# Kernel tuning notes

Hardware: AMD Instinct MI355X
Metric: run time of the kernel (lower is better)

Reference implementation:

```python
import jax, jax.numpy as jnp
import numpy as np

B, T, D = 2, 2048, 5120        # batch, seq_len, d_model
FD, E, S, K = 384, 32, 2, 2    # ffn_dim, n_experts, n_shared, top_k


def setup_inputs() -> dict:
    key = jax.random.key(0)
    ks = jax.random.split(key, 6)
    def init(k, shape, fan_in):
        return jax.random.normal(k, shape, jnp.float32) / np.sqrt(fan_in).astype(np.float32)
    return {
        "x": jax.random.normal(ks[0], (B, T, D), jnp.float32),
        "shared_w1": init(ks[1], (S, D, FD), D),
        "shared_b1": jnp.zeros((S, FD), jnp.float32),
        "shared_w2": init(ks[2], (S, FD, D), FD),
        "shared_b2": jnp.zeros((S, D), jnp.float32),
        "routed_w1": init(ks[3], (E, D, FD), D),
        "routed_b1": jnp.zeros((E, FD), jnp.float32),
        "routed_w2": init(ks[4], (E, FD, D), FD),
        "routed_b2": jnp.zeros((E, D), jnp.float32),
        "gate_w": init(ks[5], (D, E), D),
        "gate_b": jnp.zeros((E,), jnp.float32),
    }


def reference(x, shared_w1, shared_b1, shared_w2, shared_b2,
              routed_w1, routed_b1, routed_w2, routed_b2, gate_w, gate_b):
    gelu = lambda v: jax.nn.gelu(v, approximate=False)  # torch F.gelu default = exact erf

    # shared experts: sum of S dense FFNs
    h_s = gelu(jnp.einsum('btd,sdf->sbtf', x, shared_w1) + shared_b1[:, None, None, :])
    shared_out = jnp.einsum('sbtf,sfd->btd', h_s, shared_w2) + shared_b2.sum(0)

    # gating: softmax over experts, then top-k
    probs = jax.nn.softmax(x @ gate_w + gate_b, axis=-1)          # [B,T,E]
    topk_p, topk_i = jax.lax.top_k(probs, K)                      # [B,T,K]
    # dense per-(token,expert) combine weight (0 for non-selected experts)
    w_full = jnp.sum(jax.nn.one_hot(topk_i, E, dtype=x.dtype) * topk_p[..., None], axis=-2)  # [B,T,E]

    # routed experts computed densely; weights zero-out non-selected experts,
    # yielding identical math to the masked gather/scatter dispatch.
    h_r = gelu(jnp.einsum('btd,edf->ebtf', x, routed_w1) + routed_b1[:, None, None, :])
    g = h_r * jnp.transpose(w_full, (2, 0, 1))[..., None]         # fold weight pre-w2 (avoids [E,B,T,D])
    routed_out = (jnp.einsum('ebtf,efd->btd', g, routed_w2)
                  + jnp.einsum('bte,ed->btd', w_full, routed_b2))  # weighted bias term

    return shared_out + routed_out
```

## Files before the change

### kernel.cpp

```cpp
#include <hip/hip_runtime.h>
#include <math.h>

#define NTOK 4096
#define DM   5120
#define FD   384
#define NE   32

typedef float  f32x4  __attribute__((ext_vector_type(4)));
typedef __bf16 bf16x8 __attribute__((ext_vector_type(8)));
typedef unsigned short us2 __attribute__((ext_vector_type(2)));
typedef unsigned short us4 __attribute__((ext_vector_type(4)));
typedef unsigned short us8 __attribute__((ext_vector_type(8)));

__device__ __forceinline__ unsigned short f2bf(float f) {
  unsigned int u = __float_as_uint(f);
  u += 0x7fffu + ((u >> 16) & 1u);
  return (unsigned short)(u >> 16);
}

__device__ __forceinline__ float gelu_f(float v) {
  return 0.5f * v * (1.0f + erff(v * 0.70710678118654752f));
}

__device__ __forceinline__ bf16x8 ldf(const unsigned short* p) {
  us4 lo = *(const us4*)p;
  us4 hi = *(const us4*)(p + 4);
  us8 v = {lo[0], lo[1], lo[2], lo[3], hi[0], hi[1], hi[2], hi[3]};
  return __builtin_bit_cast(bf16x8, v);
}

__device__ __forceinline__ f32x4 mfma16(bf16x8 a, bf16x8 b, f32x4 c) {
  return __builtin_amdgcn_mfma_f32_16x16x32_bf16(a, b, c, 0, 0, 0);
}

__device__ __forceinline__ bf16x8 fragld(const unsigned short* t, int row, int g) {
  return *(const bf16x8*)(t + row * 64 + ((g ^ (row & 7)) << 3));
}
__device__ __forceinline__ void fragst(unsigned short* t, int row, int g, us8 v) {
  *(us8*)(t + row * 64 + ((g ^ (row & 7)) << 3)) = v;
}

#define OFF_LOGITS 0
#define OFF_COUNTS 524288
#define OFF_SEGC   524800
#define OFF_SEGB   525312
#define OFF_TABA   525824
#define OFF_TABR0  528896
#define OFF_TABR1  529920
#define OFF_TNS    530944
#define OFF_LISTS  531456
#define OFF_WLISTS 1580032
#define OFF_HBUF   2628608
#define WS_OLD     15260672UL

#define L_LOGITS 0UL
#define L_COUNTS 524288UL
#define L_HBASE  524544UL
#define L_TABA   524800UL
#define L_TABR0  527360UL
#define L_TABR1  528384UL
#define L_TNS    529408UL
#define L_LISTS  529536UL
#define L_WLIST  1578112UL
#define L_HBUF   2626688UL
#define L_XBF    15258752UL
#define L_W1T    57201792UL
#define L_W2ST   190895232UL
#define L_W2RT   198759552UL
#define WS_NEW   324588672UL

__global__ __launch_bounds__(256) void gate_v3(
    const float* __restrict__ x, const float* __restrict__ gw,
    const float* __restrict__ gb, float* __restrict__ logits,
    unsigned short* __restrict__ xbf)
{
  __shared__ __align__(16) char gsm[22656];
  float*  xs = (float*)gsm;
  float*  gs = (float*)(gsm + 4224);
  double* ps = (double*)(gsm + 4224);

  int tid = threadIdx.x;
  int t0 = blockIdx.x * 8;

  int col  = tid & 15;
  int row  = (tid >> 4) & 1;
  int part = tid >> 5;
  int e0 = col * 2;

  double a[4][2];
  #pragma unroll
  for (int i = 0; i < 4; ++i) { a[i][0] = 0.0; a[i][1] = 0.0; }

  int sx_r = tid >> 5;
  int sx_c = (tid & 31) * 4;
  const float* xg = x + (size_t)(t0 + sx_r) * DM + sx_c;
  unsigned short* xo = xbf + (size_t)(t0 + sx_r) * DM + sx_c;

  for (int k0 = 0; k0 < DM; k0 += 128) {
    float4 xv4 = *(const float4*)(xg + k0);
    *(float4*)&xs[sx_r * 132 + sx_c] = xv4;
    us4 hx = {f2bf(xv4.x), f2bf(xv4.y), f2bf(xv4.z), f2bf(xv4.w)};
    *(us4*)(xo + k0) = hx;
    #pragma unroll
    for (int p = 0; p < 4; ++p) {
      int idx = p * 256 + tid;
      int r = idx >> 3, q = (idx & 7) * 4;
      float4 g4 = *(const float4*)(gw + (size_t)(k0 + r) * NE + q);
      *(float4*)&gs[r * 36 + q] = g4;
    }
    __syncthreads();
    #pragma unroll
    for (int kk = 0; kk < 16; ++kk) {
      int k = part * 16 + kk;
      double g0 = (double)gs[k * 36 + e0];
      double g1 = (double)gs[k * 36 + e0 + 1];
      #pragma unroll
      for (int i = 0; i < 4; ++i) {
        double xv = (double)xs[(row * 4 + i) * 132 + k];
        a[i][0] = fma(xv, g0, a[i][0]);
        a[i][1] = fma(xv, g1, a[i][1]);
      }
    }
    __syncthreads();
  }

  #pragma unroll
  for (int i = 0; i < 4; ++i) {
    double2 v; v.x = a[i][0]; v.y = a[i][1];
    *(double2*)&ps[(size_t)part * 256 + (row * 4 + i) * 32 + e0] = v;
  }
  __syncthreads();
  {
    int t = tid >> 5, e = tid & 31;
    double s = 0.0;
    #pragma unroll
    for (int p = 0; p < 8; ++p) s += ps[(size_t)p * 256 + t * 32 + e];
    logits[(size_t)(t0 + t) * NE + e] = (float)s + gb[e];
  }
}

__global__ __launch_bounds__(256) void gate_logits_kernel(
    const float* __restrict__ x, const float* __restrict__ gw,
    const float* __restrict__ gb, float* __restrict__ logits,
    unsigned short* __restrict__ xbf)
{
  __shared__ float xs[16][33];
  __shared__ float gs[32][33];
  int tid = threadIdx.x;
  int t0 = blockIdx.x * 16;
  int r = tid >> 4;
  int e0 = (tid & 15) * 2;
  double a0 = 0.0, a1 = 0.0;
  for (int k0 = 0; k0 < DM; k0 += 32) {
    {
      int rr = tid >> 4, cc = (tid & 15) * 2;
      const float* s = x + (size_t)(t0 + rr) * DM + k0 + cc;
      float s0 = s[0], s1 = s[1];
      xs[rr][cc] = s0; xs[rr][cc + 1] = s1;
      if (xbf) {
        us2 h = {f2bf(s0), f2bf(s1)};
        *(us2*)(xbf + (size_t)(t0 + rr) * DM + k0 + cc) = h;
      }
    }
    {
      int rr = tid >> 3, cc = (tid & 7) * 4;
      float4 v = *(const float4*)(gw + (size_t)(k0 + rr) * NE + cc);
      gs[rr][cc] = v.x; gs[rr][cc + 1] = v.y; gs[rr][cc + 2] = v.z; gs[rr][cc + 3] = v.w;
    }
    __syncthreads();
    #pragma unroll
    for (int kk = 0; kk < 32; ++kk) {
      double a = (double)xs[r][kk];
      a0 += a * (double)gs[kk][e0];
      a1 += a * (double)gs[kk][e0 + 1];
    }
    __syncthreads();
  }
  logits[(size_t)(t0 + r) * NE + e0]     = (float)a0 + gb[e0];
  logits[(size_t)(t0 + r) * NE + e0 + 1] = (float)a1 + gb[e0 + 1];
}

__global__ void topk_kernel(const float* __restrict__ logits, int* __restrict__ counts,
                            int* __restrict__ lists, float* __restrict__ wlists)
{
  int t = blockIdx.x * blockDim.x + threadIdx.x;
  if (t >= NTOK) return;
  float l[32];
  const float4* lp = (const float4*)(logits + (size_t)t * NE);
  #pragma unroll
  for (int i = 0; i < 8; ++i) {
    float4 v = lp[i];
    l[i*4] = v.x; l[i*4+1] = v.y; l[i*4+2] = v.z; l[i*4+3] = v.w;
  }
  float mx = l[0];
  #pragma unroll
  for (int e = 1; e < 32; ++e) mx = fmaxf(mx, l[e]);
  float s = 0.f;
  #pragma unroll
  for (int e = 0; e < 32; ++e) s += expf(l[e] - mx);
  int i1 = 0; float b1 = l[0];
  #pragma unroll
  for (int e = 1; e < 32; ++e) if (l[e] > b1) { b1 = l[e]; i1 = e; }
  int i2 = -1; float b2 = -3.4e38f;
  #pragma unroll
  for (int e = 0; e < 32; ++e) if (e != i1 && l[e] > b2) { b2 = l[e]; i2 = e; }
  float p1 = expf(b1 - mx) / s;
  float p2 = expf(b2 - mx) / s;
  int pos = atomicAdd(&counts[i1], 1);
  lists [(size_t)i1 * NTOK + pos] = t;
  wlists[(size_t)i1 * NTOK + pos] = p1;
  pos = atomicAdd(&counts[32 + i2], 1);
  lists [(size_t)(32 + i2) * NTOK + pos] = t;
  wlists[(size_t)(32 + i2) * NTOK + pos] = p2;
}

__global__ void scan_kernel(const int* __restrict__ counts, int* __restrict__ seg_count,
                            int* __restrict__ seg_hbase, int2* __restrict__ tableA,
                            int2* __restrict__ tableR0, int2* __restrict__ tableR1,
                            int* __restrict__ tns)
{
  if (threadIdx.x != 0 || blockIdx.x != 0) return;
  seg_count[0] = NTOK; seg_hbase[0] = 0;
  seg_count[1] = NTOK; seg_hbase[1] = NTOK;
  int base = 2 * NTOK;
  for (int li = 0; li < 64; ++li) {
    int c = counts[li];
    seg_count[2 + li] = c; seg_hbase[2 + li] = base; base += c;
  }
  int nA = 0;
  for (int s = 0; s < 66; ++s) {
    int c = seg_count[s];
    for (int m0 = 0; m0 < c; m0 += 64) { tableA[nA].x = s; tableA[nA].y = m0; ++nA; }
  }
  int nR0 = 0;
  for (int li = 0; li < 32; ++li)
    for (int m0 = 0; m0 < counts[li]; m0 += 64) { tableR0[nR0].x = li; tableR0[nR0].y = m0; ++nR0; }
  int nR1 = 0;
  for (int li = 32; li < 64; ++li)
    for (int m0 = 0; m0 < counts[li]; m0 += 64) { tableR1[nR1].x = li; tableR1[nR1].y = m0; ++nR1; }
  tns[0] = nA; tns[1] = nR0; tns[2] = nR1;
}

__global__ __launch_bounds__(256) void ffn1_kernel(
    const float* __restrict__ x,
    const float* __restrict__ sw1, const float* __restrict__ sb1,
    const float* __restrict__ rw1, const float* __restrict__ rb1,
    const int* __restrict__ lists,
    const int* __restrict__ seg_count, const int* __restrict__ seg_hbase,
    const int2* __restrict__ tableA, const int* __restrict__ tns,
    unsigned short* __restrict__ hbuf)
{
  if ((int)blockIdx.x >= tns[0]) return;
  int2 ent = tableA[blockIdx.x];
  int seg = ent.x, m0 = ent.y;
  int cnt = seg_count[seg];
  int hbase = seg_hbase[seg];
  int n0 = blockIdx.y * 64;
  const float *w1, *b1;
  if (seg < 2) { w1 = sw1 + (size_t)seg * DM * FD; b1 = sb1 + (size_t)seg * FD; }
  else { int e = (seg - 2) & 31; w1 = rw1 + (size_t)e * DM * FD; b1 = rb1 + (size_t)e * FD; }
  __shared__ int toks[64];
  __shared__ unsigned short As[64][44];
  __shared__ unsigned short Bs[64][44];
  int tid = threadIdx.x;
  if (tid < 64) {
    int i = m0 + tid;
    int tk = 0;
    if (i < cnt) tk = (seg < 2) ? i : lists[(size_t)(seg - 2) * NTOK + i];
    toks[tid] = tk;
  }
  __syncthreads();
  int lane = tid & 63, wave = tid >> 6;
  int wr = (wave >> 1) * 32, wc = (wave & 1) * 32;
  int l15 = lane & 15, kb = (lane >> 4) * 8;
  f32x4 zz = {0.f, 0.f, 0.f, 0.f};
  f32x4 acc[2][2];
  #pragma unroll
  for (int i = 0; i < 2; ++i)
    #pragma unroll
    for (int j = 0; j < 2; ++j) acc[i][j] = zz;
  int ar = tid >> 2, ac = (tid & 3) * 8;
  const float* axp = x + (size_t)toks[ar] * DM + ac;
  int br = tid >> 3, bc = (tid & 7) * 8;
  const float* bwp = w1 + (size_t)br * FD + n0 + bc;
  for (int k0 = 0; k0 < DM; k0 += 32) {
    float4 a0 = *(const float4*)(axp + k0);
    float4 a1 = *(const float4*)(axp + k0 + 4);
    float4 w0 = *(const float4*)bwp;
    float4 w4 = *(const float4*)(bwp + 4);
    bwp += (size_t)32 * FD;
    us4 pa0 = {f2bf(a0.x), f2bf(a0.y), f2bf(a0.z), f2bf(a0.w)};
    us4 pa1 = {f2bf(a1.x), f2bf(a1.y), f2bf(a1.z), f2bf(a1.w)};
    *(us4*)&As[ar][ac] = pa0;
    *(us4*)&As[ar][ac + 4] = pa1;
    Bs[bc + 0][br] = f2bf(w0.x); Bs[bc + 1][br] = f2bf(w0.y);
    Bs[bc + 2][br] = f2bf(w0.z); Bs[bc + 3][br] = f2bf(w0.w);
    Bs[bc + 4][br] = f2bf(w4.x); Bs[bc + 5][br] = f2bf(w4.y);
    Bs[bc + 6][br] = f2bf(w4.z); Bs[bc + 7][br] = f2bf(w4.w);
    __syncthreads();
    bf16x8 af0 = ldf(&As[wr + l15][kb]);
    bf16x8 af1 = ldf(&As[wr + 16 + l15][kb]);
    bf16x8 bf0 = ldf(&Bs[wc + l15][kb]);
    bf16x8 bf1 = ldf(&Bs[wc + 16 + l15][kb]);
    acc[0][0] = mfma16(af0, bf0, acc[0][0]);
    acc[0][1] = mfma16(af0, bf1, acc[0][1]);
    acc[1][0] = mfma16(af1, bf0, acc[1][0]);
    acc[1][1] = mfma16(af1, bf1, acc[1][1]);
    __syncthreads();
  }
  int rb4 = (lane >> 4) * 4;
  #pragma unroll
  for (int mi = 0; mi < 2; ++mi) {
    #pragma unroll
    for (int rg = 0; rg < 4; ++rg) {
      int gi = m0 + wr + mi * 16 + rb4 + rg;
      if (gi < cnt) {
        #pragma unroll
        for (int ni = 0; ni < 2; ++ni) {
          int ncol = n0 + wc + ni * 16 + l15;
          float v = acc[mi][ni][rg] + b1[ncol];
          hbuf[(size_t)(hbase + gi) * FD + ncol] = f2bf(gelu_f(v));
        }
      }
    }
  }
}

__global__ __launch_bounds__(256) void ffn2_shared_kernel(
    const unsigned short* __restrict__ hbuf,
    const float* __restrict__ sw2, const float* __restrict__ sb2,
    float* __restrict__ out)
{
  int m0 = blockIdx.x * 64;
  int n0 = blockIdx.y * 64;
  __shared__ unsigned short As[64][44];
  __shared__ unsigned short Bs[64][44];
  int tid = threadIdx.x;
  int lane = tid & 63, wave = tid >> 6;
  int wr = (wave >> 1) * 32, wc = (wave & 1) * 32;
  int l15 = lane & 15, kb = (lane >> 4) * 8;
  f32x4 zz = {0.f, 0.f, 0.f, 0.f};
  f32x4 acc[2][2];
  #pragma unroll
  for (int i = 0; i < 2; ++i)
    #pragma unroll
    for (int j = 0; j < 2; ++j) acc[i][j] = zz;
  int ar = tid >> 2, ac = (tid & 3) * 8;
  int br = tid >> 3, bc = (tid & 7) * 8;
  const float* bwp = sw2 + (size_t)br * DM + n0 + bc;
  for (int k0 = 0; k0 < 2 * FD; k0 += 32) {
    int side = (k0 >= FD) ? 1 : 0;
    const unsigned short* ap =
        hbuf + (size_t)(side * NTOK + m0 + ar) * FD + (k0 - side * FD) + ac;
    us8 av = *(const us8*)ap;
    float4 w0 = *(const float4*)bwp;
    float4 w4 = *(const float4*)(bwp + 4);
    bwp += (size_t)32 * DM;
    us4 alo = {av[0], av[1], av[2], av[3]};
    us4 ahi = {av[4], av[5], av[6], av[7]};
    *(us4*)&As[ar][ac] = alo;
    *(us4*)&As[ar][ac + 4] = ahi;
    Bs[bc + 0][br] = f2bf(w0.x); Bs[bc + 1][br] = f2bf(w0.y);
    Bs[bc + 2][br] = f2bf(w0.z); Bs[bc + 3][br] = f2bf(w0.w);
    Bs[bc + 4][br] = f2bf(w4.x); Bs[bc + 5][br] = f2bf(w4.y);
    Bs[bc + 6][br] = f2bf(w4.z); Bs[bc + 7][br] = f2bf(w4.w);
    __syncthreads();
    bf16x8 af0 = ldf(&As[wr + l15][kb]);
    bf16x8 af1 = ldf(&As[wr + 16 + l15][kb]);
    bf16x8 bf0 = ldf(&Bs[wc + l15][kb]);
    bf16x8 bf1 = ldf(&Bs[wc + 16 + l15][kb]);
    acc[0][0] = mfma16(af0, bf0, acc[0][0]);
    acc[0][1] = mfma16(af0, bf1, acc[0][1]);
    acc[1][0] = mfma16(af1, bf0, acc[1][0]);
    acc[1][1] = mfma16(af1, bf1, acc[1][1]);
    __syncthreads();
  }
  int rb4 = (lane >> 4) * 4;
  #pragma unroll
  for (int mi = 0; mi < 2; ++mi) {
    #pragma unroll
    for (int rg = 0; rg < 4; ++rg) {
      int row = m0 + wr + mi * 16 + rb4 + rg;
      #pragma unroll
      for (int ni = 0; ni < 2; ++ni) {
        int ncol = n0 + wc + ni * 16 + l15;
        out[(size_t)row * DM + ncol] = acc[mi][ni][rg] + sb2[ncol] + sb2[DM + ncol];
      }
    }
  }
}

__global__ __launch_bounds__(256) void ffn2_routed_kernel(
    const unsigned short* __restrict__ hbuf,
    const float* __restrict__ rw2, const float* __restrict__ rb2,
    const int* __restrict__ lists, const float* __restrict__ wlists,
    const int* __restrict__ counts, const int* __restrict__ seg_hbase,
    const int2* __restrict__ tableR, const int* __restrict__ tns, int tidx,
    float* __restrict__ out)
{
  if ((int)blockIdx.x >= tns[tidx]) return;
  int2 ent = tableR[blockIdx.x];
  int li = ent.x, m0 = ent.y;
  int cnt = counts[li];
  int hbase = seg_hbase[2 + li];
  int e = li & 31;
  int n0 = blockIdx.y * 64;
  const float* w2 = rw2 + (size_t)e * FD * DM;
  const float* b2 = rb2 + (size_t)e * DM;
  __shared__ unsigned short As[64][44];
  __shared__ unsigned short Bs[64][44];
  int tid = threadIdx.x;
  int lane = tid & 63, wave = tid >> 6;
  int wr = (wave >> 1) * 32, wc = (wave & 1) * 32;
  int l15 = lane & 15, kb = (lane >> 4) * 8;
  f32x4 zz = {0.f, 0.f, 0.f, 0.f};
  f32x4 acc[2][2];
  #pragma unroll
  for (int i = 0; i < 2; ++i)
    #pragma unroll
    for (int j = 0; j < 2; ++j) acc[i][j] = zz;
  int ar = tid >> 2, ac = (tid & 3) * 8;
  const unsigned short* ap = hbuf + (size_t)(hbase + m0 + ar) * FD + ac;
  int br = tid >> 3, bc = (tid & 7) * 8;
  const float* bwp = w2 + (size_t)br * DM + n0 + bc;
  for (int k0 = 0; k0 < FD; k0 += 32) {
    us8 av = *(const us8*)(ap + k0);
    float4 w0 = *(const float4*)bwp;
    float4 w4 = *(const float4*)(bwp + 4);
    bwp += (size_t)32 * DM;
    us4 alo = {av[0], av[1], av[2], av[3]};
    us4 ahi = {av[4], av[5], av[6], av[7]};
    *(us4*)&As[ar][ac] = alo;
    *(us4*)&As[ar][ac + 4] = ahi;
    Bs[bc + 0][br] = f2bf(w0.x); Bs[bc + 1][br] = f2bf(w0.y);
    Bs[bc + 2][br] = f2bf(w0.z); Bs[bc + 3][br] = f2bf(w0.w);
    Bs[bc + 4][br] = f2bf(w4.x); Bs[bc + 5][br] = f2bf(w4.y);
    Bs[bc + 6][br] = f2bf(w4.z); Bs[bc + 7][br] = f2bf(w4.w);
    __syncthreads();
    bf16x8 af0 = ldf(&As[wr + l15][kb]);
    bf16x8 af1 = ldf(&As[wr + 16 + l15][kb]);
    bf16x8 bf0 = ldf(&Bs[wc + l15][kb]);
    bf16x8 bf1 = ldf(&Bs[wc + 16 + l15][kb]);
    acc[0][0] = mfma16(af0, bf0, acc[0][0]);
    acc[0][1] = mfma16(af0, bf1, acc[0][1]);
    acc[1][0] = mfma16(af1, bf0, acc[1][0]);
    acc[1][1] = mfma16(af1, bf1, acc[1][1]);
    __syncthreads();
  }
  int rb4 = (lane >> 4) * 4;
  #pragma unroll
  for (int mi = 0; mi < 2; ++mi) {
    #pragma unroll
    for (int rg = 0; rg < 4; ++rg) {
      int gi = m0 + wr + mi * 16 + rb4 + rg;
      if (gi < cnt) {
        int tok = lists[(size_t)li * NTOK + gi];
        float wgt = wlists[(size_t)li * NTOK + gi];
        #pragma unroll
        for (int ni = 0; ni < 2; ++ni) {
          int ncol = n0 + wc + ni * 16 + l15;
          float v = (acc[mi][ni][rg] + b2[ncol]) * wgt;
          out[(size_t)tok * DM + ncol] += v;
        }
      }
    }
  }
}


__global__ void scan_v3(const int* __restrict__ counts, int* __restrict__ hbase_g,
                        int2* __restrict__ tableA, int2* __restrict__ tableR0,
                        int2* __restrict__ tableR1, int* __restrict__ tns)
{
  __shared__ int cnt[64], tprefA[64], tpref0[32], tpref1[32], hpref[64];
  int t = threadIdx.x;
  if (t < 64) cnt[t] = counts[t];
  __syncthreads();
  if (t == 0) {
    int hb = 2 * NTOK, ta = 128, t0 = 0, t1 = 0;
    for (int i = 0; i < 64; ++i) {
      int nt = (cnt[i] + 63) >> 6;
      hpref[i] = hb; hb += cnt[i];
      tprefA[i] = ta; ta += nt;
      if (i < 32) { tpref0[i] = t0; t0 += nt; }
      else        { tpref1[i - 32] = t1; t1 += nt; }
    }
    tns[0] = ta; tns[1] = t0; tns[2] = t1;
  }
  __syncthreads();
  if (t < 128) {
    int2 ent; ent.x = t >> 6; ent.y = (t & 63) * 64;
    tableA[t] = ent;
  }
  if (t < 64) {
    hbase_g[t] = hpref[t];
    int nt = (cnt[t] + 63) >> 6;
    for (int j = 0; j < nt; ++j) {
      int2 ent; ent.x = 2 + t; ent.y = j * 64;
      tableA[tprefA[t] + j] = ent;
      int2 entR; entR.x = t; entR.y = j * 64;
      if (t < 32) tableR0[tpref0[t] + j] = entR;
      else        tableR1[tpref1[t - 32] + j] = entR;
    }
  }
}

__global__ __launch_bounds__(256) void conv_w1_v2(
    const float* __restrict__ sw1, const float* __restrict__ rw1,
    unsigned short* __restrict__ w1T)
{
  int seg = blockIdx.x;
  int k0 = blockIdx.y * 64;
  int n0 = blockIdx.z * 64;
  const float* src = (seg < 2) ? sw1 + (size_t)seg * DM * FD
                               : rw1 + (size_t)(seg - 2) * DM * FD;
  __shared__ float ls[64][68];
  int tid = threadIdx.x;
  int r = tid >> 4, c4 = (tid & 15) * 4;
  #pragma unroll
  for (int p = 0; p < 4; ++p) {
    float4 v = *(const float4*)(src + (size_t)(k0 + r + p * 16) * FD + n0 + c4);
    *(float4*)&ls[r + p * 16][c4] = v;
  }
  __syncthreads();
  int n = tid >> 2, kseg = (tid & 3) * 16;
  unsigned short tmp[16];
  #pragma unroll
  for (int j = 0; j < 16; ++j) tmp[j] = f2bf(ls[kseg + j][n]);
  unsigned short* dst = w1T + (size_t)seg * FD * DM + (size_t)(n0 + n) * DM + k0 + kseg;
  us8 o0 = {tmp[0], tmp[1], tmp[2], tmp[3], tmp[4], tmp[5], tmp[6], tmp[7]};
  us8 o1 = {tmp[8], tmp[9], tmp[10], tmp[11], tmp[12], tmp[13], tmp[14], tmp[15]};
  *(us8*)dst = o0;
  *(us8*)(dst + 8) = o1;
}

__global__ __launch_bounds__(256) void conv_w2_v2(
    const float* __restrict__ sw2, const float* __restrict__ rw2,
    unsigned short* __restrict__ w2sT, unsigned short* __restrict__ w2rT)
{
  int e = blockIdx.x;
  int K = (e == 0) ? 2 * FD : FD;
  int k0 = blockIdx.y * 64;
  if (k0 >= K) return;
  int n0 = blockIdx.z * 64;
  const float* src = (e == 0) ? sw2 : rw2 + (size_t)(e - 1) * FD * DM;
  unsigned short* dstb = (e == 0) ? w2sT : w2rT + (size_t)(e - 1) * DM * FD;
  __shared__ float ls[64][68];
  int tid = threadIdx.x;
  int r = tid >> 4, c4 = (tid & 15) * 4;
  #pragma unroll
  for (int p = 0; p < 4; ++p) {
    float4 v = *(const float4*)(src + (size_t)(k0 + r + p * 16) * DM + n0 + c4);
    *(float4*)&ls[r + p * 16][c4] = v;
  }
  __syncthreads();
  int n = tid >> 2, kseg = (tid & 3) * 16;
  unsigned short tmp[16];
  #pragma unroll
  for (int j = 0; j < 16; ++j) tmp[j] = f2bf(ls[kseg + j][n]);
  unsigned short* dst = dstb + (size_t)(n0 + n) * K + k0 + kseg;
  us8 o0 = {tmp[0], tmp[1], tmp[2], tmp[3], tmp[4], tmp[5], tmp[6], tmp[7]};
  us8 o1 = {tmp[8], tmp[9], tmp[10], tmp[11], tmp[12], tmp[13], tmp[14], tmp[15]};
  *(us8*)dst = o0;
  *(us8*)(dst + 8) = o1;
}

__global__ __launch_bounds__(256) void ffn1_v3(
    const unsigned short* __restrict__ xbf, const unsigned short* __restrict__ w1T,
    const float* __restrict__ sb1, const float* __restrict__ rb1,
    const int* __restrict__ lists, const int* __restrict__ counts,
    const int* __restrict__ hbase_g, const int2* __restrict__ tableA,
    const int* __restrict__ tns, unsigned short* __restrict__ hbuf)
{
  if ((int)blockIdx.x >= tns[0]) return;
  int2 ent = tableA[blockIdx.x];
  int seg = ent.x, m0 = ent.y;
  int cnt, hbase, wseg;
  const float* b1;
  if (seg < 2) {
    cnt = NTOK; hbase = seg * NTOK; b1 = sb1 + seg * FD; wseg = seg;
  } else {
    int li = seg - 2;
    int e = li & 31;
    cnt = counts[li]; hbase = hbase_g[li];
    b1 = rb1 + (size_t)e * FD;
    wseg = 2 + e;
  }
  int n0 = blockIdx.y * 128;
  const unsigned short* w1 = w1T + (size_t)wseg * FD * DM;

  __shared__ int toks[64];
  __shared__ __align__(16) unsigned short As[64 * 64];
  __shared__ __align__(16) unsigned short Bs[128 * 64];

  int tid = threadIdx.x;
  if (tid < 64) {
    int i = m0 + tid;
    int tk;
    if (seg < 2) tk = (i < cnt) ? i : 0;
    else tk = (i < cnt) ? lists[(size_t)(seg - 2) * NTOK + i] : 0;
    toks[tid] = tk;
  }
  __syncthreads();

  int lane = tid & 63, wave = tid >> 6;
  int wr = (wave >> 1) * 32, wc = (wave & 1) * 64;
  int l15 = lane & 15, l4 = lane >> 4;

  f32x4 zz = {0.f, 0.f, 0.f, 0.f};
  f32x4 acc[2][4];
  #pragma unroll
  for (int i = 0; i < 2; ++i)
    #pragma unroll
    for (int j = 0; j < 4; ++j) acc[i][j] = zz;

  int ar0 = tid >> 3, ag0 = tid & 7;
  int arw[2] = {ar0, 32 + ar0};
  const unsigned short* asrc[2];
  asrc[0] = xbf + (size_t)toks[arw[0]] * DM + ag0 * 8;
  asrc[1] = xbf + (size_t)toks[arw[1]] * DM + ag0 * 8;
  const unsigned short* bsrc[4];
  int brow[4];
  #pragma unroll
  for (int p = 0; p < 4; ++p) {
    int idx = p * 256 + tid;
    brow[p] = idx >> 3;
    bsrc[p] = w1 + (size_t)(n0 + brow[p]) * DM + (idx & 7) * 8;
  }

  for (int k0 = 0; k0 < DM; k0 += 64) {
    us8 va[2], vb[4];
    #pragma unroll
    for (int p = 0; p < 2; ++p) va[p] = *(const us8*)(asrc[p] + k0);
    #pragma unroll
    for (int p = 0; p < 4; ++p) vb[p] = *(const us8*)(bsrc[p] + k0);
    #pragma unroll
    for (int p = 0; p < 2; ++p) fragst(As, arw[p], ag0, va[p]);
    #pragma unroll
    for (int p = 0; p < 4; ++p) fragst(Bs, brow[p], ag0, vb[p]);
    __syncthreads();
    #pragma unroll
    for (int kk = 0; kk < 2; ++kk) {
      bf16x8 af[2], bfr[4];
      #pragma unroll
      for (int mi = 0; mi < 2; ++mi) af[mi] = fragld(As, wr + mi * 16 + l15, kk * 4 + l4);
      #pragma unroll
      for (int ni = 0; ni < 4; ++ni) bfr[ni] = fragld(Bs, wc + ni * 16 + l15, kk * 4 + l4);
      #pragma unroll
      for (int mi = 0; mi < 2; ++mi)
        #pragma unroll
        for (int ni = 0; ni < 4; ++ni) acc[mi][ni] = mfma16(af[mi], bfr[ni], acc[mi][ni]);
    }
    __syncthreads();
  }

  int rb4 = l4 * 4;
  #pragma unroll
  for (int mi = 0; mi < 2; ++mi) {
    #pragma unroll
    for (int rg = 0; rg < 4; ++rg) {
      int gi = m0 + wr + mi * 16 + rb4 + rg;
      if (gi < cnt) {
        #pragma unroll
        for (int ni = 0; ni < 4; ++ni) {
          int ncol = n0 + wc + ni * 16 + l15;
          float v = acc[mi][ni][rg] + b1[ncol];
          hbuf[(size_t)(hbase + gi) * FD + ncol] = f2bf(gelu_f(v));
        }
      }
    }
  }
}

__global__ __launch_bounds__(256) void ffn2_shared_v2(
    const unsigned short* __restrict__ hbuf, const unsigned short* __restrict__ w2sT,
    const float* __restrict__ sb2, float* __restrict__ out)
{
  int m0 = blockIdx.x * 128;
  int n0 = blockIdx.y * 128;

  __shared__ __align__(16) unsigned short As[128 * 64];
  __shared__ __align__(16) unsigned short Bs[128 * 64];

  int tid = threadIdx.x;
  int lane = tid & 63, wave = tid >> 6;
  int wr = (wave >> 1) * 64, wc = (wave & 1) * 64;
  int l15 = lane & 15, l4 = lane >> 4;

  f32x4 zz = {0.f, 0.f, 0.f, 0.f};
  f32x4 acc[4][4];
  #pragma unroll
  for (int i = 0; i < 4; ++i)
    #pragma unroll
    for (int j = 0; j < 4; ++j) acc[i][j] = zz;

  int prow[4], pg[4];
  #pragma unroll
  for (int p = 0; p < 4; ++p) {
    int idx = p * 256 + tid;
    prow[p] = idx >> 3; pg[p] = idx & 7;
  }

  for (int k0 = 0; k0 < 2 * FD; k0 += 64) {
    int side = (k0 >= FD) ? 1 : 0;
    int kk0 = k0 - side * FD;
    us8 va[4], vb[4];
    #pragma unroll
    for (int p = 0; p < 4; ++p)
      va[p] = *(const us8*)(hbuf + (size_t)(side * NTOK + m0 + prow[p]) * FD + kk0 + pg[p] * 8);
    #pragma unroll
    for (int p = 0; p < 4; ++p)
      vb[p] = *(const us8*)(w2sT + (size_t)(n0 + prow[p]) * (2 * FD) + k0 + pg[p] * 8);
    #pragma unroll
    for (int p = 0; p < 4; ++p) fragst(As, prow[p], pg[p], va[p]);
    #pragma unroll
    for (int p = 0; p < 4; ++p) fragst(Bs, prow[p], pg[p], vb[p]);
    __syncthreads();
    #pragma unroll
    for (int kk = 0; kk < 2; ++kk) {
      bf16x8 af[4], bfr[4];
      #pragma unroll
      for (int mi = 0; mi < 4; ++mi) af[mi] = fragld(As, wr + mi * 16 + l15, kk * 4 + l4);
      #pragma unroll
      for (int ni = 0; ni < 4; ++ni) bfr[ni] = fragld(Bs, wc + ni * 16 + l15, kk * 4 + l4);
      #pragma unroll
      for (int mi = 0; mi < 4; ++mi)
        #pragma unroll
        for (int ni = 0; ni < 4; ++ni) acc[mi][ni] = mfma16(af[mi], bfr[ni], acc[mi][ni]);
    }
    __syncthreads();
  }

  int rb4 = l4 * 4;
  #pragma unroll
  for (int mi = 0; mi < 4; ++mi) {
    #pragma unroll
    for (int rg = 0; rg < 4; ++rg) {
      int row = m0 + wr + mi * 16 + rb4 + rg;
      #pragma unroll
      for (int ni = 0; ni < 4; ++ni) {
        int ncol = n0 + wc + ni * 16 + l15;
        out[(size_t)row * DM + ncol] = acc[mi][ni][rg] + sb2[ncol] + sb2[DM + ncol];
      }
    }
  }
}

__global__ __launch_bounds__(256) void ffn2_routed_v2(
    const unsigned short* __restrict__ hbuf, const unsigned short* __restrict__ w2rT,
    const float* __restrict__ rb2, const int* __restrict__ lists,
    const float* __restrict__ wlists, const int* __restrict__ counts,
    const int* __restrict__ hbase_g, const int2* __restrict__ tableR,
    const int* __restrict__ tns, int tidx, float* __restrict__ out)
{
  if ((int)blockIdx.x >= tns[tidx]) return;
  int2 ent = tableR[blockIdx.x];
  int li = ent.x, m0 = ent.y;
  int cnt = counts[li];
  int hbase = hbase_g[li];
  int e = li & 31;
  int n0 = blockIdx.y * 128;
  const unsigned short* w2 = w2rT + (size_t)e * DM * FD;

  __shared__ __align__(16) unsigned short As[64 * 64];
  __shared__ __align__(16) unsigned short Bs[128 * 64];

  int tid = threadIdx.x;
  int lane = tid & 63, wave = tid >> 6;
  int wr = (wave >> 1) * 32, wc = (wave & 1) * 64;
  int l15 = lane & 15, l4 = lane >> 4;

  f32x4 zz = {0.f, 0.f, 0.f, 0.f};
  f32x4 acc[2][4];
  #pragma unroll
  for (int i = 0; i < 2; ++i)
    #pragma unroll
    for (int j = 0; j < 4; ++j) acc[i][j] = zz;

  int ar0 = tid >> 3, ag0 = tid & 7;
  int arw[2] = {ar0, 32 + ar0};
  const unsigned short* asrc[2];
  asrc[0] = hbuf + (size_t)(hbase + m0 + arw[0]) * FD + ag0 * 8;
  asrc[1] = hbuf + (size_t)(hbase + m0 + arw[1]) * FD + ag0 * 8;
  const unsigned short* bsrc[4];
  int brow[4];
  #pragma unroll
  for (int p = 0; p < 4; ++p) {
    int idx = p * 256 + tid;
    brow[p] = idx >> 3;
    bsrc[p] = w2 + (size_t)(n0 + brow[p]) * FD + (idx & 7) * 8;
  }

  for (int k0 = 0; k0 < FD; k0 += 64) {
    us8 va[2], vb[4];
    #pragma unroll
    for (int p = 0; p < 2; ++p) va[p] = *(const us8*)(asrc[p] + k0);
    #pragma unroll
    for (int p = 0; p < 4; ++p) vb[p] = *(const us8*)(bsrc[p] + k0);
    #pragma unroll
    for (int p = 0; p < 2; ++p) fragst(As, arw[p], ag0, va[p]);
    #pragma unroll
    for (int p = 0; p < 4; ++p) fragst(Bs, brow[p], ag0, vb[p]);
    __syncthreads();
    #pragma unroll
    for (int kk = 0; kk < 2; ++kk) {
      bf16x8 af[2], bfr[4];
      #pragma unroll
      for (int mi = 0; mi < 2; ++mi) af[mi] = fragld(As, wr + mi * 16 + l15, kk * 4 + l4);
      #pragma unroll
      for (int ni = 0; ni < 4; ++ni) bfr[ni] = fragld(Bs, wc + ni * 16 + l15, kk * 4 + l4);
      #pragma unroll
      for (int mi = 0; mi < 2; ++mi)
        #pragma unroll
        for (int ni = 0; ni < 4; ++ni) acc[mi][ni] = mfma16(af[mi], bfr[ni], acc[mi][ni]);
    }
    __syncthreads();
  }

  int rb4 = l4 * 4;
  #pragma unroll
  for (int mi = 0; mi < 2; ++mi) {
    #pragma unroll
    for (int rg = 0; rg < 4; ++rg) {
      int gi = m0 + wr + mi * 16 + rb4 + rg;
      if (gi < cnt) {
        int tok = lists[(size_t)li * NTOK + gi];
        float wgt = wlists[(size_t)li * NTOK + gi];
        #pragma unroll
        for (int ni = 0; ni < 4; ++ni) {
          int ncol = n0 + wc + ni * 16 + l15;
          float v = (acc[mi][ni][rg] + rb2[(size_t)e * DM + ncol]) * wgt;
          out[(size_t)tok * DM + ncol] += v;
        }
      }
    }
  }
}

extern "C" void kernel_launch(void* const* d_in, const int* in_sizes, int n_in,
                              void* d_out, int out_size, void* d_ws, size_t ws_size,
                              hipStream_t stream) {
  const float* x   = (const float*)d_in[0];
  const float* sw1 = (const float*)d_in[1];
  const float* sb1 = (const float*)d_in[2];
  const float* sw2 = (const float*)d_in[3];
  const float* sb2 = (const float*)d_in[4];
  const float* rw1 = (const float*)d_in[5];
  const float* rb1 = (const float*)d_in[6];
  const float* rw2 = (const float*)d_in[7];
  const float* rb2 = (const float*)d_in[8];
  const float* gw  = (const float*)d_in[9];
  const float* gb  = (const float*)d_in[10];
  float* out = (float*)d_out;
  char* ws = (char*)d_ws;

  if (ws_size >= WS_NEW) {
    float* logits  = (float*)(ws + L_LOGITS);
    int* counts    = (int*)(ws + L_COUNTS);
    int* hbase_g   = (int*)(ws + L_HBASE);
    int2* tableA   = (int2*)(ws + L_TABA);
    int2* tableR0  = (int2*)(ws + L_TABR0);
    int2* tableR1  = (int2*)(ws + L_TABR1);
    int* tns       = (int*)(ws + L_TNS);
    int* lists     = (int*)(ws + L_LISTS);
    float* wlists  = (float*)(ws + L_WLIST);
    unsigned short* hbuf = (unsigned short*)(ws + L_HBUF);
    unsigned short* xbf  = (unsigned short*)(ws + L_XBF);
    unsigned short* w1T  = (unsigned short*)(ws + L_W1T);
    unsigned short* w2sT = (unsigned short*)(ws + L_W2ST);
    unsigned short* w2rT = (unsigned short*)(ws + L_W2RT);

    hipMemsetAsync(counts, 0, 64 * sizeof(int), stream);
    gate_v3<<<dim3(NTOK / 8), 256, 0, stream>>>(x, gw, gb, logits, xbf);
    topk_kernel<<<dim3(NTOK / 256), 256, 0, stream>>>(logits, counts, lists, wlists);
    scan_v3<<<1, 128, 0, stream>>>(counts, hbase_g, tableA, tableR0, tableR1, tns);
    conv_w1_v2<<<dim3(34, 80, 6), 256, 0, stream>>>(sw1, rw1, w1T);
    conv_w2_v2<<<dim3(33, 12, 80), 256, 0, stream>>>(sw2, rw2, w2sT, w2rT);
    ffn1_v3<<<dim3(320, 3), 256, 0, stream>>>(xbf, w1T, sb1, rb1, lists, counts,
                                              hbase_g, tableA, tns, hbuf);
    ffn2_shared_v2<<<dim3(32, 40), 256, 0, stream>>>(hbuf, w2sT, sb2, out);
    ffn2_routed_v2<<<dim3(128, 40), 256, 0, stream>>>(hbuf, w2rT, rb2, lists, wlists,
                                                      counts, hbase_g, tableR0, tns, 1, out);
    ffn2_routed_v2<<<dim3(128, 40), 256, 0, stream>>>(hbuf, w2rT, rb2, lists, wlists,
                                                      counts, hbase_g, tableR1, tns, 2, out);
    return;
  }

  if (ws_size < WS_OLD) return;
  float* logits   = (float*)(ws + OFF_LOGITS);
  int* counts     = (int*)(ws + OFF_COUNTS);
  int* seg_count  = (int*)(ws + OFF_SEGC);
  int* seg_hbase  = (int*)(ws + OFF_SEGB);
  int2* tableA    = (int2*)(ws + OFF_TABA);
  int2* tableR0   = (int2*)(ws + OFF_TABR0);
  int2* tableR1   = (int2*)(ws + OFF_TABR1);
  int* tns        = (int*)(ws + OFF_TNS);
  int* lists      = (int*)(ws + OFF_LISTS);
  float* wlists   = (float*)(ws + OFF_WLISTS);
  unsigned short* hbuf = (unsigned short*)(ws + OFF_HBUF);

  hipMemsetAsync(counts, 0, 64 * sizeof(int), stream);
  gate_logits_kernel<<<dim3(NTOK / 16), 256, 0, stream>>>(x, gw, gb, logits, (unsigned short*)0);
  topk_kernel<<<dim3(NTOK / 256), 256, 0, stream>>>(logits, counts, lists, wlists);
  scan_kernel<<<1, 1, 0, stream>>>(counts, seg_count, seg_hbase, tableA, tableR0, tableR1, tns);
  ffn1_kernel<<<dim3(384, 6), 256, 0, stream>>>(x, sw1, sb1, rw1, rb1, lists,
                                                seg_count, seg_hbase, tableA, tns, hbuf);
  ffn2_shared_kernel<<<dim3(64, 80), 256, 0, stream>>>(hbuf, sw2, sb2, out);
  ffn2_routed_kernel<<<dim3(128, 80), 256, 0, stream>>>(hbuf, rw2, rb2, lists, wlists,
                                                        counts, seg_hbase, tableR0, tns, 1, out);
  ffn2_routed_kernel<<<dim3(128, 80), 256, 0, stream>>>(hbuf, rw2, rb2, lists, wlists,
                                                        counts, seg_hbase, tableR1, tns, 2, out);
}
```

Measured before the change: 654.4 us.

## Double-buffer LDS tiles in FFN GEMMs and swizzle weight-conversion transposes

The three GEMM kernels (ffn1, shared ffn2, routed ffn2) now keep two LDS buffers. Each loop iteration issues the global loads for the next k-tile before the MFMA work on the current tile, then writes them to the other buffer, so each iteration needs one barrier instead of two. This is meant to hide global-load latency behind compute. The weight conversion kernels also XOR-swizzle the LDS transpose columns to reduce bank conflicts on the column reads. In exchange, LDS use doubles (up to 64KB in the shared ffn2 kernel), which may lower occupancy.

```diff
diff --git a/kernel.cpp b/kernel.cpp
--- a/kernel.cpp
+++ b/kernel.cpp
@@ -519,14 +519,16 @@
   int r = tid >> 4, c4 = (tid & 15) * 4;
   #pragma unroll
   for (int p = 0; p < 4; ++p) {
-    float4 v = *(const float4*)(src + (size_t)(k0 + r + p * 16) * FD + n0 + c4);
-    *(float4*)&ls[r + p * 16][c4] = v;
+    int row = r + p * 16;
+    float4 v = *(const float4*)(src + (size_t)(k0 + row) * FD + n0 + c4);
+    *(float4*)&ls[row][c4 ^ (((row >> 4) & 3) << 4)] = v;
   }
   __syncthreads();
   int n = tid >> 2, kseg = (tid & 3) * 16;
+  int swz = ((kseg >> 4) & 3) << 4;
   unsigned short tmp[16];
   #pragma unroll
-  for (int j = 0; j < 16; ++j) tmp[j] = f2bf(ls[kseg + j][n]);
+  for (int j = 0; j < 16; ++j) tmp[j] = f2bf(ls[kseg + j][n ^ swz]);
   unsigned short* dst = w1T + (size_t)seg * FD * DM + (size_t)(n0 + n) * DM + k0 + kseg;
   us8 o0 = {tmp[0], tmp[1], tmp[2], tmp[3], tmp[4], tmp[5], tmp[6], tmp[7]};
   us8 o1 = {tmp[8], tmp[9], tmp[10], tmp[11], tmp[12], tmp[13], tmp[14], tmp[15]};
@@ -550,14 +552,16 @@
   int r = tid >> 4, c4 = (tid & 15) * 4;
   #pragma unroll
   for (int p = 0; p < 4; ++p) {
-    float4 v = *(const float4*)(src + (size_t)(k0 + r + p * 16) * DM + n0 + c4);
-    *(float4*)&ls[r + p * 16][c4] = v;
+    int row = r + p * 16;
+    float4 v = *(const float4*)(src + (size_t)(k0 + row) * DM + n0 + c4);
+    *(float4*)&ls[row][c4 ^ (((row >> 4) & 3) << 4)] = v;
   }
   __syncthreads();
   int n = tid >> 2, kseg = (tid & 3) * 16;
+  int swz = ((kseg >> 4) & 3) << 4;
   unsigned short tmp[16];
   #pragma unroll
-  for (int j = 0; j < 16; ++j) tmp[j] = f2bf(ls[kseg + j][n]);
+  for (int j = 0; j < 16; ++j) tmp[j] = f2bf(ls[kseg + j][n ^ swz]);
   unsigned short* dst = dstb + (size_t)(n0 + n) * K + k0 + kseg;
   us8 o0 = {tmp[0], tmp[1], tmp[2], tmp[3], tmp[4], tmp[5], tmp[6], tmp[7]};
   us8 o1 = {tmp[8], tmp[9], tmp[10], tmp[11], tmp[12], tmp[13], tmp[14], tmp[15]};
@@ -590,8 +594,8 @@
   const unsigned short* w1 = w1T + (size_t)wseg * FD * DM;
 
   __shared__ int toks[64];
-  __shared__ __align__(16) unsigned short As[64 * 64];
-  __shared__ __align__(16) unsigned short Bs[128 * 64];
+  __shared__ __align__(16) unsigned short As[2][64 * 64];
+  __shared__ __align__(16) unsigned short Bs[2][128 * 64];
 
   int tid = threadIdx.x;
   if (tid < 64) {
@@ -628,30 +632,53 @@
     bsrc[p] = w1 + (size_t)(n0 + brow[p]) * DM + (idx & 7) * 8;
   }
 
+  {
+    us8 va[2], vb[4];
+    #pragma unroll
+    for (int p = 0; p < 2; ++p) va[p] = *(const us8*)(asrc[p]);
+    #pragma unroll
+    for (int p = 0; p < 4; ++p) vb[p] = *(const us8*)(bsrc[p]);
+    #pragma unroll
+    for (int p = 0; p < 2; ++p) fragst(As[0], arw[p], ag0, va[p]);
+    #pragma unroll
+    for (int p = 0; p < 4; ++p) fragst(Bs[0], brow[p], ag0, vb[p]);
+  }
+  __syncthreads();
+
+  int cur = 0;
   for (int k0 = 0; k0 < DM; k0 += 64) {
-    us8 va[2], vb[4];
-    #pragma unroll
-    for (int p = 0; p < 2; ++p) va[p] = *(const us8*)(asrc[p] + k0);
-    #pragma unroll
-    for (int p = 0; p < 4; ++p) vb[p] = *(const us8*)(bsrc[p] + k0);
-    #pragma unroll
-    for (int p = 0; p < 2; ++p) fragst(As, arw[p], ag0, va[p]);
-    #pragma unroll
-    for (int p = 0; p < 4; ++p) fragst(Bs, brow[p], ag0, vb[p]);
-    __syncthreads();
+    int nk = k0 + 64;
+    us8 va1[2], vb1[4];
+    if (nk < DM) {
+      #pragma unroll
+      for (int p = 0; p < 2; ++p) va1[p] = *(const us8*)(asrc[p] + nk);
+      #pragma unroll
+      for (int p = 0; p < 4; ++p) vb1[p] = *(const us8*)(bsrc[p] + nk);
+    }
+    const unsigned short* Ac = As[cur];
+    const unsigned short* Bc = Bs[cur];
     #pragma unroll
     for (int kk = 0; kk < 2; ++kk) {
       bf16x8 af[2], bfr[4];
       #pragma unroll
-      for (int mi = 0; mi < 2; ++mi) af[mi] = fragld(As, wr + mi * 16 + l15, kk * 4 + l4);
-      #pragma unroll
-      for (int ni = 0; ni < 4; ++ni) bfr[ni] = fragld(Bs, wc + ni * 16 + l15, kk * 4 + l4);
+      for (int mi = 0; mi < 2; ++mi) af[mi] = fragld(Ac, wr + mi * 16 + l15, kk * 4 + l4);
+      #pragma unroll
+      for (int ni = 0; ni < 4; ++ni) bfr[ni] = fragld(Bc, wc + ni * 16 + l15, kk * 4 + l4);
       #pragma unroll
       for (int mi = 0; mi < 2; ++mi)
         #pragma unroll
         for (int ni = 0; ni < 4; ++ni) acc[mi][ni] = mfma16(af[mi], bfr[ni], acc[mi][ni]);
     }
-    __syncthreads();
+    if (nk < DM) {
+      unsigned short* An = As[cur ^ 1];
+      unsigned short* Bn = Bs[cur ^ 1];
+      #pragma unroll
+      for (int p = 0; p < 2; ++p) fragst(An, arw[p], ag0, va1[p]);
+      #pragma unroll
+      for (int p = 0; p < 4; ++p) fragst(Bn, brow[p], ag0, vb1[p]);
+    }
+    __syncthreads();
+    cur ^= 1;
   }
 
   int rb4 = l4 * 4;
@@ -679,8 +706,8 @@
   int m0 = blockIdx.x * 128;
   int n0 = blockIdx.y * 128;
 
-  __shared__ __align__(16) unsigned short As[128 * 64];
-  __shared__ __align__(16) unsigned short Bs[128 * 64];
+  __shared__ __align__(16) unsigned short As[2][128 * 64];
+  __shared__ __align__(16) unsigned short Bs[2][128 * 64];
 
   int tid = threadIdx.x;
   int lane = tid & 63, wave = tid >> 6;
@@ -701,34 +728,59 @@
     prow[p] = idx >> 3; pg[p] = idx & 7;
   }
 
+  {
+    us8 va[4], vb[4];
+    #pragma unroll
+    for (int p = 0; p < 4; ++p)
+      va[p] = *(const us8*)(hbuf + (size_t)(m0 + prow[p]) * FD + pg[p] * 8);
+    #pragma unroll
+    for (int p = 0; p < 4; ++p)
+      vb[p] = *(const us8*)(w2sT + (size_t)(n0 + prow[p]) * (2 * FD) + pg[p] * 8);
+    #pragma unroll
+    for (int p = 0; p < 4; ++p) fragst(As[0], prow[p], pg[p], va[p]);
+    #pragma unroll
+    for (int p = 0; p < 4; ++p) fragst(Bs[0], prow[p], pg[p], vb[p]);
+  }
+  __syncthreads();
+
+  int cur = 0;
   for (int k0 = 0; k0 < 2 * FD; k0 += 64) {
-    int side = (k0 >= FD) ? 1 : 0;
-    int kk0 = k0 - side * FD;
-    us8 va[4], vb[4];
-    #pragma unroll
-    for (int p = 0; p < 4; ++p)
-      va[p] = *(const us8*)(hbuf + (size_t)(side * NTOK + m0 + prow[p]) * FD + kk0 + pg[p] * 8);
-    #pragma unroll
-    for (int p = 0; p < 4; ++p)
-      vb[p] = *(const us8*)(w2sT + (size_t)(n0 + prow[p]) * (2 * FD) + k0 + pg[p] * 8);
-    #pragma unroll
-    for (int p = 0; p < 4; ++p) fragst(As, prow[p], pg[p], va[p]);
-    #pragma unroll
-    for (int p = 0; p < 4; ++p) fragst(Bs, prow[p], pg[p], vb[p]);
-    __syncthreads();
+    int nk = k0 + 64;
+    us8 va1[4], vb1[4];
+    if (nk < 2 * FD) {
+      int side = (nk >= FD) ? 1 : 0;
+      int kk0 = nk - side * FD;
+      #pragma unroll
+      for (int p = 0; p < 4; ++p)
+        va1[p] = *(const us8*)(hbuf + (size_t)(side * NTOK + m0 + prow[p]) * FD + kk0 + pg[p] * 8);
+      #pragma unroll
+      for (int p = 0; p < 4; ++p)
+        vb1[p] = *(const us8*)(w2sT + (size_t)(n0 + prow[p]) * (2 * FD) + nk + pg[p] * 8);
+    }
+    const unsigned short* Ac = As[cur];
+    const unsigned short* Bc = Bs[cur];
     #pragma unroll
     for (int kk = 0; kk < 2; ++kk) {
       bf16x8 af[4], bfr[4];
       #pragma unroll
-      for (int mi = 0; mi < 4; ++mi) af[mi] = fragld(As, wr + mi * 16 + l15, kk * 4 + l4);
-      #pragma unroll
-      for (int ni = 0; ni < 4; ++ni) bfr[ni] = fragld(Bs, wc + ni * 16 + l15, kk * 4 + l4);
+      for (int mi = 0; mi < 4; ++mi) af[mi] = fragld(Ac, wr + mi * 16 + l15, kk * 4 + l4);
+      #pragma unroll
+      for (int ni = 0; ni < 4; ++ni) bfr[ni] = fragld(Bc, wc + ni * 16 + l15, kk * 4 + l4);
       #pragma unroll
       for (int mi = 0; mi < 4; ++mi)
         #pragma unroll
         for (int ni = 0; ni < 4; ++ni) acc[mi][ni] = mfma16(af[mi], bfr[ni], acc[mi][ni]);
     }
-    __syncthreads();
+    if (nk < 2 * FD) {
+      unsigned short* An = As[cur ^ 1];
+      unsigned short* Bn = Bs[cur ^ 1];
+      #pragma unroll
+      for (int p = 0; p < 4; ++p) fragst(An, prow[p], pg[p], va1[p]);
+      #pragma unroll
+      for (int p = 0; p < 4; ++p) fragst(Bn, prow[p], pg[p], vb1[p]);
+    }
+    __syncthreads();
+    cur ^= 1;
   }
 
   int rb4 = l4 * 4;
@@ -762,8 +814,8 @@
   int n0 = blockIdx.y * 128;
   const unsigned short* w2 = w2rT + (size_t)e * DM * FD;
 
-  __shared__ __align__(16) unsigned short As[64 * 64];
-  __shared__ __align__(16) unsigned short Bs[128 * 64];
+  __shared__ __align__(16) unsigned short As[2][64 * 64];
+  __shared__ __align__(16) unsigned short Bs[2][128 * 64];
 
   int tid = threadIdx.x;
   int lane = tid & 63, wave = tid >> 6;
@@ -791,30 +843,53 @@
     bsrc[p] = w2 + (size_t)(n0 + brow[p]) * FD + (idx & 7) * 8;
   }
 
+  {
+    us8 va[2], vb[4];
+    #pragma unroll
+    for (int p = 0; p < 2; ++p) va[p] = *(const us8*)(asrc[p]);
+    #pragma unroll
+    for (int p = 0; p < 4; ++p) vb[p] = *(const us8*)(bsrc[p]);
+    #pragma unroll
+    for (int p = 0; p < 2; ++p) fragst(As[0], arw[p], ag0, va[p]);
+    #pragma unroll
+    for (int p = 0; p < 4; ++p) fragst(Bs[0], brow[p], ag0, vb[p]);
+  }
+  __syncthreads();
+
+  int cur = 0;
   for (int k0 = 0; k0 < FD; k0 += 64) {
-    us8 va[2], vb[4];
-    #pragma unroll
-    for (int p = 0; p < 2; ++p) va[p] = *(const us8*)(asrc[p] + k0);
-    #pragma unroll
-    for (int p = 0; p < 4; ++p) vb[p] = *(const us8*)(bsrc[p] + k0);
-    #pragma unroll
-    for (int p = 0; p < 2; ++p) fragst(As, arw[p], ag0, va[p]);
-    #pragma unroll
-    for (int p = 0; p < 4; ++p) fragst(Bs, brow[p], ag0, vb[p]);
-    __syncthreads();
+    int nk = k0 + 64;
+    us8 va1[2], vb1[4];
+    if (nk < FD) {
+      #pragma unroll
+      for (int p = 0; p < 2; ++p) va1[p] = *(const us8*)(asrc[p] + nk);
+      #pragma unroll
+      for (int p = 0; p < 4; ++p) vb1[p] = *(const us8*)(bsrc[p] + nk);
+    }
+    const unsigned short* Ac = As[cur];
+    const unsigned short* Bc = Bs[cur];
     #pragma unroll
     for (int kk = 0; kk < 2; ++kk) {
       bf16x8 af[2], bfr[4];
       #pragma unroll
-      for (int mi = 0; mi < 2; ++mi) af[mi] = fragld(As, wr + mi * 16 + l15, kk * 4 + l4);
-      #pragma unroll
-      for (int ni = 0; ni < 4; ++ni) bfr[ni] = fragld(Bs, wc + ni * 16 + l15, kk * 4 + l4);
+      for (int mi = 0; mi < 2; ++mi) af[mi] = fragld(Ac, wr + mi * 16 + l15, kk * 4 + l4);
+      #pragma unroll
+      for (int ni = 0; ni < 4; ++ni) bfr[ni] = fragld(Bc, wc + ni * 16 + l15, kk * 4 + l4);
       #pragma unroll
       for (int mi = 0; mi < 2; ++mi)
         #pragma unroll
         for (int ni = 0; ni < 4; ++ni) acc[mi][ni] = mfma16(af[mi], bfr[ni], acc[mi][ni]);
     }
-    __syncthreads();
+    if (nk < FD) {
+      unsigned short* An = As[cur ^ 1];
+      unsigned short* Bn = Bs[cur ^ 1];
+      #pragma unroll
+      for (int p = 0; p < 2; ++p) fragst(An, arw[p], ag0, va1[p]);
+      #pragma unroll
+      for (int p = 0; p < 4; ++p) fragst(Bn, brow[p], ag0, vb1[p]);
+    }
+    __syncthreads();
+    cur ^= 1;
   }
 
   int rb4 = l4 * 4;
```

Result: slower. 689.3 us (+5.3%).

## Load GEMM tiles directly into LDS and swizzle transpose staging buffers

Applied to the files above, without the earlier changes.

The three GEMM kernels (ffn1, shared ffn2, routed ffn2) now stage A and B tiles with global_load_lds 16-byte direct-to-LDS loads instead of loading into registers and then storing to LDS. The XOR swizzle is moved to the global source address so the existing fragment reads still match. The weight-conversion transpose kernels also gain an XOR swizzle on their fp32 LDS tile to reduce bank conflicts on column reads. This is meant to cut VGPR pressure and LDS store instructions, but it relies on the builtin's per-wave destination layout being correct and still synchronises with barriers and no explicit vmcnt wait.

```diff
diff --git a/kernel.cpp b/kernel.cpp
--- a/kernel.cpp
+++ b/kernel.cpp
@@ -38,6 +38,12 @@
 }
 __device__ __forceinline__ void fragst(unsigned short* t, int row, int g, us8 v) {
   *(us8*)(t + row * 64 + ((g ^ (row & 7)) << 3)) = v;
+}
+
+__device__ __forceinline__ void gld16(const void* g, void* l) {
+  __builtin_amdgcn_global_load_lds(
+      (const __attribute__((address_space(1))) unsigned int*)g,
+      (__attribute__((address_space(3))) unsigned int*)l, 16, 0, 0);
 }
 
 #define OFF_LOGITS 0
@@ -519,14 +525,16 @@
   int r = tid >> 4, c4 = (tid & 15) * 4;
   #pragma unroll
   for (int p = 0; p < 4; ++p) {
-    float4 v = *(const float4*)(src + (size_t)(k0 + r + p * 16) * FD + n0 + c4);
-    *(float4*)&ls[r + p * 16][c4] = v;
+    int row = r + p * 16;
+    float4 v = *(const float4*)(src + (size_t)(k0 + row) * FD + n0 + c4);
+    *(float4*)&ls[row][c4 ^ (((row >> 4) & 3) << 4)] = v;
   }
   __syncthreads();
   int n = tid >> 2, kseg = (tid & 3) * 16;
+  int swz = ((kseg >> 4) & 3) << 4;
   unsigned short tmp[16];
   #pragma unroll
-  for (int j = 0; j < 16; ++j) tmp[j] = f2bf(ls[kseg + j][n]);
+  for (int j = 0; j < 16; ++j) tmp[j] = f2bf(ls[kseg + j][n ^ swz]);
   unsigned short* dst = w1T + (size_t)seg * FD * DM + (size_t)(n0 + n) * DM + k0 + kseg;
   us8 o0 = {tmp[0], tmp[1], tmp[2], tmp[3], tmp[4], tmp[5], tmp[6], tmp[7]};
   us8 o1 = {tmp[8], tmp[9], tmp[10], tmp[11], tmp[12], tmp[13], tmp[14], tmp[15]};
@@ -550,14 +558,16 @@
   int r = tid >> 4, c4 = (tid & 15) * 4;
   #pragma unroll
   for (int p = 0; p < 4; ++p) {
-    float4 v = *(const float4*)(src + (size_t)(k0 + r + p * 16) * DM + n0 + c4);
-    *(float4*)&ls[r + p * 16][c4] = v;
+    int row = r + p * 16;
+    float4 v = *(const float4*)(src + (size_t)(k0 + row) * DM + n0 + c4);
+    *(float4*)&ls[row][c4 ^ (((row >> 4) & 3) << 4)] = v;
   }
   __syncthreads();
   int n = tid >> 2, kseg = (tid & 3) * 16;
+  int swz = ((kseg >> 4) & 3) << 4;
   unsigned short tmp[16];
   #pragma unroll
-  for (int j = 0; j < 16; ++j) tmp[j] = f2bf(ls[kseg + j][n]);
+  for (int j = 0; j < 16; ++j) tmp[j] = f2bf(ls[kseg + j][n ^ swz]);
   unsigned short* dst = dstb + (size_t)(n0 + n) * K + k0 + kseg;
   us8 o0 = {tmp[0], tmp[1], tmp[2], tmp[3], tmp[4], tmp[5], tmp[6], tmp[7]};
   us8 o1 = {tmp[8], tmp[9], tmp[10], tmp[11], tmp[12], tmp[13], tmp[14], tmp[15]};
@@ -614,30 +624,27 @@
     #pragma unroll
     for (int j = 0; j < 4; ++j) acc[i][j] = zz;
 
-  int ar0 = tid >> 3, ag0 = tid & 7;
-  int arw[2] = {ar0, 32 + ar0};
-  const unsigned short* asrc[2];
-  asrc[0] = xbf + (size_t)toks[arw[0]] * DM + ag0 * 8;
-  asrc[1] = xbf + (size_t)toks[arw[1]] * DM + ag0 * 8;
-  const unsigned short* bsrc[4];
-  int brow[4];
+  int g = lane & 7, lr = lane >> 3;
+  int arow[2];  const unsigned short* agsrc[2];  unsigned short* aldst[2];
+  #pragma unroll
+  for (int p = 0; p < 2; ++p) {
+    arow[p] = wave * 16 + p * 8 + lr;
+    agsrc[p] = xbf + (size_t)toks[arow[p]] * DM + ((g ^ (arow[p] & 7)) << 3);
+    aldst[p] = As + (wave * 16 + p * 8) * 64;
+  }
+  int brow[4];  const unsigned short* bgsrc[4];  unsigned short* bldst[4];
   #pragma unroll
   for (int p = 0; p < 4; ++p) {
-    int idx = p * 256 + tid;
-    brow[p] = idx >> 3;
-    bsrc[p] = w1 + (size_t)(n0 + brow[p]) * DM + (idx & 7) * 8;
+    brow[p] = wave * 32 + p * 8 + lr;
+    bgsrc[p] = w1 + (size_t)(n0 + brow[p]) * DM + ((g ^ (brow[p] & 7)) << 3);
+    bldst[p] = Bs + (wave * 32 + p * 8) * 64;
   }
 
   for (int k0 = 0; k0 < DM; k0 += 64) {
-    us8 va[2], vb[4];
-    #pragma unroll
-    for (int p = 0; p < 2; ++p) va[p] = *(const us8*)(asrc[p] + k0);
-    #pragma unroll
-    for (int p = 0; p < 4; ++p) vb[p] = *(const us8*)(bsrc[p] + k0);
-    #pragma unroll
-    for (int p = 0; p < 2; ++p) fragst(As, arw[p], ag0, va[p]);
-    #pragma unroll
-    for (int p = 0; p < 4; ++p) fragst(Bs, brow[p], ag0, vb[p]);
+    #pragma unroll
+    for (int p = 0; p < 2; ++p) gld16(agsrc[p] + k0, aldst[p]);
+    #pragma unroll
+    for (int p = 0; p < 4; ++p) gld16(bgsrc[p] + k0, bldst[p]);
     __syncthreads();
     #pragma unroll
     for (int kk = 0; kk < 2; ++kk) {
@@ -694,27 +701,27 @@
     #pragma unroll
     for (int j = 0; j < 4; ++j) acc[i][j] = zz;
 
-  int prow[4], pg[4];
+  int g = lane & 7, lr = lane >> 3;
+  int prow[4];  unsigned short* aldst[4];  unsigned short* bldst[4];
+  const unsigned short* bgsrc[4];
+  int aswz[4];
   #pragma unroll
   for (int p = 0; p < 4; ++p) {
-    int idx = p * 256 + tid;
-    prow[p] = idx >> 3; pg[p] = idx & 7;
+    prow[p] = wave * 32 + p * 8 + lr;
+    aldst[p] = As + (wave * 32 + p * 8) * 64;
+    bldst[p] = Bs + (wave * 32 + p * 8) * 64;
+    aswz[p] = (g ^ (prow[p] & 7)) << 3;
+    bgsrc[p] = w2sT + (size_t)(n0 + prow[p]) * (2 * FD) + aswz[p];
   }
 
   for (int k0 = 0; k0 < 2 * FD; k0 += 64) {
     int side = (k0 >= FD) ? 1 : 0;
     int kk0 = k0 - side * FD;
-    us8 va[4], vb[4];
     #pragma unroll
     for (int p = 0; p < 4; ++p)
-      va[p] = *(const us8*)(hbuf + (size_t)(side * NTOK + m0 + prow[p]) * FD + kk0 + pg[p] * 8);
-    #pragma unroll
-    for (int p = 0; p < 4; ++p)
-      vb[p] = *(const us8*)(w2sT + (size_t)(n0 + prow[p]) * (2 * FD) + k0 + pg[p] * 8);
-    #pragma unroll
-    for (int p = 0; p < 4; ++p) fragst(As, prow[p], pg[p], va[p]);
-    #pragma unroll
-    for (int p = 0; p < 4; ++p) fragst(Bs, prow[p], pg[p], vb[p]);
+      gld16(hbuf + (size_t)(side * NTOK + m0 + prow[p]) * FD + kk0 + aswz[p], aldst[p]);
+    #pragma unroll
+    for (int p = 0; p < 4; ++p) gld16(bgsrc[p] + k0, bldst[p]);
     __syncthreads();
     #pragma unroll
     for (int kk = 0; kk < 2; ++kk) {
@@ -777,30 +784,27 @@
     #pragma unroll
     for (int j = 0; j < 4; ++j) acc[i][j] = zz;
 
-  int ar0 = tid >> 3, ag0 = tid & 7;
-  int arw[2] = {ar0, 32 + ar0};
-  const unsigned short* asrc[2];
-  asrc[0] = hbuf + (size_t)(hbase + m0 + arw[0]) * FD + ag0 * 8;
-  asrc[1] = hbuf + (size_t)(hbase + m0 + arw[1]) * FD + ag0 * 8;
-  const unsigned short* bsrc[4];
-  int brow[4];
+  int g = lane & 7, lr = lane >> 3;
+  const unsigned short* agsrc[2];  unsigned short* aldst[2];
+  #pragma unroll
+  for (int p = 0; p < 2; ++p) {
+    int arow = wave * 16 + p * 8 + lr;
+    agsrc[p] = hbuf + (size_t)(hbase + m0 + arow) * FD + ((g ^ (arow & 7)) << 3);
+    aldst[p] = As + (wave * 16 + p * 8) * 64;
+  }
+  const unsigned short* bgsrc[4];  unsigned short* bldst[4];
   #pragma unroll
   for (int p = 0; p < 4; ++p) {
-    int idx = p * 256 + tid;
-    brow[p] = idx >> 3;
-    bsrc[p] = w2 + (size_t)(n0 + brow[p]) * FD + (idx & 7) * 8;
+    int brow = wave * 32 + p * 8 + lr;
+    bgsrc[p] = w2 + (size_t)(n0 + brow) * FD + ((g ^ (brow & 7)) << 3);
+    bldst[p] = Bs + (wave * 32 + p * 8) * 64;
   }
 
   for (int k0 = 0; k0 < FD; k0 += 64) {
-    us8 va[2], vb[4];
-    #pragma unroll
-    for (int p = 0; p < 2; ++p) va[p] = *(const us8*)(asrc[p] + k0);
-    #pragma unroll
-    for (int p = 0; p < 4; ++p) vb[p] = *(const us8*)(bsrc[p] + k0);
-    #pragma unroll
-    for (int p = 0; p < 2; ++p) fragst(As, arw[p], ag0, va[p]);
-    #pragma unroll
-    for (int p = 0; p < 4; ++p) fragst(Bs, brow[p], ag0, vb[p]);
+    #pragma unroll
+    for (int p = 0; p < 2; ++p) gld16(agsrc[p] + k0, aldst[p]);
+    #pragma unroll
+    for (int p = 0; p < 4; ++p) gld16(bgsrc[p] + k0, bldst[p]);
     __syncthreads();
     #pragma unroll
     for (int kk = 0; kk < 2; ++kk) {
```

Result: no change. 646.0 us (-1.3%).
